# Kernel tuning notes

Hardware: AMD Instinct MI355X
Metric: run time of the kernel (lower is better)

## Reference

```python
import jax, jax.numpy as jnp
import numpy as np

V, D, C, H = 32, 128, 2048, 8
B, M = 8, 2048
HD = D // H


def rms_norm(x, scale):
    # Whole-tensor (per-batch) RMS over dims (1,2), as in the source (quirky but faithful).
    Bx, Mx, Dx = x.shape
    fr = jnp.sqrt(jnp.sum(x * x, axis=(1, 2))) * (Mx * Dx) ** -0.5  # (B,)
    raw = x / fr[:, None, None]
    return scale[:Mx, :][None, :, :] * raw


def rope_tables(Mx):
    i = jnp.arange(D // 2, dtype=jnp.float32)
    # NOTE: faithful to source: exponent uses (i-1), not i.
    base = jnp.power(10000.0, -2.0 * (i - 1.0) / D)  # (D/2,)
    pos = jnp.arange(Mx, dtype=jnp.float32)
    ang = pos[:, None] * base[None, :]  # (M, D/2)
    return jnp.cos(ang), jnp.sin(ang)


def apply_rope(t, cos, sin):
    # Equivalent to bmm with the block-diagonal 2x2 rotation matrices:
    # out[2i]   =  t[2i]*cos + t[2i+1]*sin
    # out[2i+1] = -t[2i]*sin + t[2i+1]*cos
    te, to = t[..., 0::2], t[..., 1::2]
    oe = te * cos + to * sin
    oo = -te * sin + to * cos
    return jnp.stack([oe, oo], axis=-1).reshape(t.shape)


def mha(q, k, v, in_w, in_b, out_w, out_b):
    Bx, Mx, _ = q.shape
    qp = q @ in_w[:D].T + in_b[:D]
    kp = k @ in_w[D:2 * D].T + in_b[D:2 * D]
    vp = v @ in_w[2 * D:].T + in_b[2 * D:]
    qh = qp.reshape(Bx, Mx, H, HD).transpose(0, 2, 1, 3)
    kh = kp.reshape(Bx, Mx, H, HD).transpose(0, 2, 1, 3)
    vh = vp.reshape(Bx, Mx, H, HD).transpose(0, 2, 1, 3)
    scores = jnp.einsum('bhqd,bhkd->bhqk', qh, kh) / jnp.sqrt(jnp.float32(HD))
    causal = jnp.tril(jnp.ones((Mx, Mx), dtype=bool))
    scores = jnp.where(causal[None, None], scores, -jnp.inf)
    probs = jax.nn.softmax(scores, axis=-1)  # dropout=0.1 in train mode; eval here
    o = jnp.einsum('bhqk,bhkd->bhqd', probs, vh)
    o = o.transpose(0, 2, 1, 3).reshape(Bx, Mx, D)
    return o @ out_w.T + out_b


def setup_inputs():
    key = jax.random.key(0)
    ks = jax.random.split(key, 12)
    s = 0.02
    return {
        'idx': jax.random.randint(ks[0], (B, M), 0, V),
        'targets': jax.random.randint(ks[1], (B, M), 0, V),
        'emb': jax.random.normal(ks[2], (V, D), jnp.float32) * s,
        'rms_scale': jnp.ones((C, D), jnp.float32),
        'Wq': jax.random.normal(ks[3], (D, D), jnp.float32) * s,
        'Wk': jax.random.normal(ks[4], (D, D), jnp.float32) * s,
        'Wv': jax.random.normal(ks[5], (D, D), jnp.float32) * s,
        'in_proj_w': jax.random.normal(ks[6], (3 * D, D), jnp.float32) * s,
        'in_proj_b': jnp.zeros((3 * D,), jnp.float32),
        'out_proj_w': jax.random.normal(ks[7], (D, D), jnp.float32) * s,
        'out_proj_b': jnp.zeros((D,), jnp.float32),
        'lin_w': jax.random.normal(ks[8], (D, D), jnp.float32) * s,
        'lin_b': jnp.zeros((D,), jnp.float32),
        'out_w': jax.random.normal(ks[9], (V, D), jnp.float32) * s,
        'out_b': jnp.zeros((V,), jnp.float32),
    }


def reference(idx, targets, emb, rms_scale, Wq, Wk, Wv, in_proj_w, in_proj_b,
              out_proj_w, out_proj_b, lin_w, lin_b, out_w, out_b):
    x = emb[idx]                                  # (B, M, D)
    x = rms_norm(x, rms_scale)
    Q = x @ Wq.T
    K = x @ Wk.T
    Vv = x @ Wv.T
    cos, sin = rope_tables(x.shape[1])
    q_out = apply_rope(Q, cos, sin)
    k_out = apply_rope(K, cos, sin)
    v_out = apply_rope(Vv, cos, sin)              # source rotates V too (faithful)
    x = x + mha(q_out, k_out, v_out, in_proj_w, in_proj_b, out_proj_w, out_proj_b)
    x = rms_norm(x, rms_scale)
    x = x + jax.nn.relu(x @ lin_w.T + lin_b)
    logits = x @ out_w.T + out_b                  # (B, M, V)
    logp = jax.nn.log_softmax(logits, axis=-1)
    nll = -jnp.take_along_axis(logp, targets[..., None], axis=-1)[..., 0]
    loss = jnp.mean(nll)
    return logits, loss
```

## Files before the change

kernel.cpp:

```cpp
#include <hip/hip_runtime.h>
#include <hip/hip_bf16.h>
#include <math.h>

#define Vv   32
#define Dd   128
#define Hh   8
#define Bb   8
#define Mm   2048
#define BM   (Bb*Mm)
#define NEL  (BM*Dd)
#define XNS  140
#define QKS  396

typedef _Float16 half4_t __attribute__((ext_vector_type(4)));
typedef _Float16 half8_t __attribute__((ext_vector_type(8)));
typedef __fp16   fp16x2  __attribute__((ext_vector_type(2)));
typedef float    float4_t __attribute__((ext_vector_type(4)));
#define MFMA16 __builtin_amdgcn_mfma_f32_16x16x16f16
#define MFMA32 __builtin_amdgcn_mfma_f32_16x16x32_f16

#if __has_builtin(__builtin_amdgcn_exp2f)
__device__ __forceinline__ float fexp2(float x) { return __builtin_amdgcn_exp2f(x); }
#else
__device__ __forceinline__ float fexp2(float x) { return __expf(x * 0.6931471805599453f); }
#endif

__global__ __launch_bounds__(256) void front_kernel(const float* __restrict__ Wq,
                                                    const float* __restrict__ Wk,
                                                    const float* __restrict__ Wv,
                                                    const float* __restrict__ in_w,
                                                    const float* __restrict__ out_pw,
                                                    const float* __restrict__ lin_w,
                                                    const float* __restrict__ out_w,
                                                    _Float16* __restrict__ Wh,
                                                    float* __restrict__ cosT,
                                                    float* __restrict__ sinT,
                                                    const int* __restrict__ idx,
                                                    const float* __restrict__ emb,
                                                    _Float16* __restrict__ Xh,
                                                    float* __restrict__ partials,
                                                    float* __restrict__ lossOut) {
    __shared__ float wsum[4];
    if (blockIdx.x < 1040) {
        if (blockIdx.x == 0 && threadIdx.x == 0) lossOut[0] = 0.f;
        int gid = blockIdx.x * 256 + threadIdx.x;
        if (gid < 135168) {
            const float* src;
            int i;
            if (gid < 131072) {
                int seg = gid >> 14; i = gid & 16383;
                src = seg == 0 ? Wq : seg == 1 ? Wk : seg == 2 ? Wv :
                      seg < 6 ? in_w + (size_t)(seg - 3) * 16384 :
                      seg == 6 ? out_pw : lin_w;
            } else { src = out_w; i = gid - 131072; }
            int tile = i >> 8, within = i & 255;
            int nt = tile >> 3, kk = tile & 7;
            int r = within >> 4, cc = within & 15;
            Wh[gid] = (_Float16)src[(nt * 16 + r) * 128 + kk * 16 + cc];
        } else {
            int rid = gid - 135168;
            int i = rid & 63, m = rid >> 6;
            float ex = -2.0f * ((float)i - 1.0f) / 128.0f;
            float basef = expf(ex * 9.210340371976184f);
            float ang = (float)m * basef;
            cosT[rid] = cosf(ang);
            sinT[rid] = sinf(ang);
        }
    } else {
        int blk = blockIdx.x - 1040;
        int gid = blk * 256 + threadIdx.x;
        int token = gid >> 5, t4 = gid & 31;
        float4 x = *(const float4*)(emb + (size_t)idx[token] * 128 + t4 * 4);
        half4_t o;
        o[0] = (_Float16)x.x; o[1] = (_Float16)x.y; o[2] = (_Float16)x.z; o[3] = (_Float16)x.w;
        *(half4_t*)(Xh + (size_t)gid * 4) = o;
        float v = x.x * x.x + x.y * x.y + x.z * x.z + x.w * x.w;
        #pragma unroll
        for (int off = 32; off; off >>= 1) v += __shfl_xor(v, off);
        int lane = threadIdx.x & 63, wave = threadIdx.x >> 6;
        if (lane == 0) wsum[wave] = v;
        __syncthreads();
        if (threadIdx.x == 0) partials[blk] = wsum[0] + wsum[1] + wsum[2] + wsum[3];
    }
}

__global__ __launch_bounds__(512, 4) void gemm_qkvproj_kernel(const _Float16* __restrict__ xh,
                                                              const float* __restrict__ scale,
                                                              const float* __restrict__ part1,
                                                              const _Float16* __restrict__ Whqkv,
                                                              const _Float16* __restrict__ Whin,
                                                              const float* __restrict__ in_b,
                                                              const float* __restrict__ cosT,
                                                              const float* __restrict__ sinT,
                                                              _Float16* __restrict__ xnh,
                                                              _Float16* __restrict__ Qp,
                                                              _Float16* __restrict__ Kp,
                                                              _Float16* __restrict__ Vp) {
    __shared__ _Float16 xn[32 * XNS];
    __shared__ _Float16 qkv[32 * QKS];
    __shared__ float wsum0[8];
    int tid = threadIdx.x;
    int row0 = blockIdx.x * 32;
    {
        float v = (tid < 256) ? part1[(row0 >> 11) * 256 + tid] : 0.f;
        #pragma unroll
        for (int off = 32; off; off >>= 1) v += __shfl_xor(v, off);
        if ((tid & 63) == 0) wsum0[tid >> 6] = v;
    }
    __syncthreads();
    float iv = 512.0f / sqrtf(((wsum0[0] + wsum0[1]) + (wsum0[2] + wsum0[3])) +
                              ((wsum0[4] + wsum0[5]) + (wsum0[6] + wsum0[7])));
    {
        int rw = tid >> 4, c8 = (tid & 15) * 8;
        int m = (row0 + rw) & (Mm - 1);
        half8_t x8 = *(const half8_t*)(xh + (size_t)(row0 + rw) * 128 + c8);
        const float* sp = scale + (size_t)m * 128 + c8;
        float4 s0 = *(const float4*)sp;
        float4 s1 = *(const float4*)(sp + 4);
        half8_t o8;
        o8[0] = (_Float16)((float)x8[0] * iv * s0.x);
        o8[1] = (_Float16)((float)x8[1] * iv * s0.y);
        o8[2] = (_Float16)((float)x8[2] * iv * s0.z);
        o8[3] = (_Float16)((float)x8[3] * iv * s0.w);
        o8[4] = (_Float16)((float)x8[4] * iv * s1.x);
        o8[5] = (_Float16)((float)x8[5] * iv * s1.y);
        o8[6] = (_Float16)((float)x8[6] * iv * s1.z);
        o8[7] = (_Float16)((float)x8[7] * iv * s1.w);
        *(half8_t*)(xn + rw * XNS + c8) = o8;
        *(half8_t*)(xnh + (size_t)(row0 + rw) * 128 + c8) = o8;
    }
    __syncthreads();
    int wave = tid >> 6, lane = tid & 63;
    int r = lane & 15, c = lane >> 4;
    int nb = wave * 48;
    int aoff = c * 8;
    int boff = r * 16 + (c & 1) * 8;
    int bsel = c >> 1;
    {
        float4_t acc[2][3];
        #pragma unroll
        for (int rt = 0; rt < 2; rt++)
            #pragma unroll
            for (int t = 0; t < 3; t++) acc[rt][t] = (float4_t){0.f, 0.f, 0.f, 0.f};
        #pragma unroll
        for (int kk = 0; kk < 4; kk++) {
            half8_t a0 = *(const half8_t*)(xn + r * XNS + kk * 32 + aoff);
            half8_t a1 = *(const half8_t*)(xn + (16 + r) * XNS + kk * 32 + aoff);
            half8_t wf[3];
            #pragma unroll
            for (int t = 0; t < 3; t++)
                wf[t] = *(const half8_t*)(Whqkv + ((wave * 3 + t) * 8 + kk * 2 + bsel) * 256 + boff);
            #pragma unroll
            for (int t = 0; t < 3; t++) {
                acc[0][t] = MFMA32(a0, wf[t], acc[0][t], 0, 0, 0);
                acc[1][t] = MFMA32(a1, wf[t], acc[1][t], 0, 0, 0);
            }
        }
        #pragma unroll
        for (int rt = 0; rt < 2; rt++) {
            #pragma unroll
            for (int t = 0; t < 3; t++) {
                int n = nb + t * 16 + r;
                int ci = (n & 127) >> 1;
                #pragma unroll
                for (int reg = 0; reg < 4; reg++) {
                    int m2 = (row0 + rt * 16 + 4 * c + reg) & (Mm - 1);
                    float v = acc[rt][t][reg];
                    float vp = __shfl_xor(v, 1);
                    float cs = cosT[m2 * 64 + ci], sn = sinT[m2 * 64 + ci];
                    v = (n & 1) ? (-vp * sn + v * cs) : (v * cs + vp * sn);
                    qkv[(rt * 16 + 4 * c + reg) * QKS + n] = (_Float16)v;
                }
            }
        }
    }
    __syncthreads();
    {
        int seg_lo = nb >> 7;
        int seg_hi = (nb + 32) >> 7;
        float4_t acc[2][3];
        #pragma unroll
        for (int rt = 0; rt < 2; rt++)
            #pragma unroll
            for (int t = 0; t < 3; t++) acc[rt][t] = (float4_t){0.f, 0.f, 0.f, 0.f};
        #pragma unroll
        for (int kk = 0; kk < 4; kk++) {
            half8_t al0 = *(const half8_t*)(qkv + r * QKS + seg_lo * 128 + kk * 32 + aoff);
            half8_t al1 = *(const half8_t*)(qkv + (16 + r) * QKS + seg_lo * 128 + kk * 32 + aoff);
            half8_t ah0 = *(const half8_t*)(qkv + r * QKS + seg_hi * 128 + kk * 32 + aoff);
            half8_t ah1 = *(const half8_t*)(qkv + (16 + r) * QKS + seg_hi * 128 + kk * 32 + aoff);
            #pragma unroll
            for (int t = 0; t < 3; t++) {
                int colg = nb + t * 16;
                int seg = colg >> 7;
                int ntl = (colg & 127) >> 4;
                half8_t wf = *(const half8_t*)(Whin + ((seg * 8 + ntl) * 8 + kk * 2 + bsel) * 256 + boff);
                bool lo = (seg == seg_lo);
                acc[0][t] = MFMA32(lo ? al0 : ah0, wf, acc[0][t], 0, 0, 0);
                acc[1][t] = MFMA32(lo ? al1 : ah1, wf, acc[1][t], 0, 0, 0);
            }
        }
        int bb = row0 >> 11;
        #pragma unroll
        for (int rt = 0; rt < 2; rt++) {
            int t16 = ((row0 + rt * 16) & 2047) >> 4;
            #pragma unroll
            for (int t = 0; t < 3; t++) {
                int colg = nb + t * 16;
                int seg = colg >> 7;
                int h = (colg & 127) >> 4;
                size_t tb = ((size_t)(bb * 8 + h) * 128 + t16) * 256;
                float bv = in_b[colg + r];
                _Float16* dst = seg == 0 ? Qp : seg == 1 ? Kp : Vp;
                #pragma unroll
                for (int reg = 0; reg < 4; reg++) {
                    float v = acc[rt][t][reg] + bv;
                    int key = 4 * c + reg;
                    if (seg < 2) dst[tb + key * 16 + r] = (_Float16)v;
                    else         dst[tb + r * 16 + key] = (_Float16)v;
                }
            }
        }
    }
}

__global__ __launch_bounds__(512, 4) void gemm_ep1_kernel(const _Float16* __restrict__ Oh,
                                                          const _Float16* __restrict__ W6,
                                                          const float* __restrict__ bias,
                                                          const _Float16* __restrict__ xnh,
                                                          _Float16* __restrict__ xresh,
                                                          float* __restrict__ partials) {
    __shared__ _Float16 At[32 * XNS];
    int tid = threadIdx.x;
    int row0 = blockIdx.x * 32;
    {
        int rw = tid >> 4, c8 = (tid & 15) * 8;
        *(half8_t*)(At + rw * XNS + c8) = *(const half8_t*)(Oh + (size_t)(row0 + rw) * 128 + c8);
    }
    __syncthreads();
    int wave = tid >> 6, lane = tid & 63;
    int r = lane & 15, c = lane >> 4;
    int aoff = c * 8;
    int boff = r * 16 + (c & 1) * 8;
    int bsel = c >> 1;
    int n0 = wave * 16;
    float4_t acc[2];
    acc[0] = (float4_t){0.f, 0.f, 0.f, 0.f};
    acc[1] = (float4_t){0.f, 0.f, 0.f, 0.f};
    #pragma unroll
    for (int kk = 0; kk < 4; kk++) {
        half8_t a0 = *(const half8_t*)(At + r * XNS + kk * 32 + aoff);
        half8_t a1 = *(const half8_t*)(At + (16 + r) * XNS + kk * 32 + aoff);
        half8_t wf = *(const half8_t*)(W6 + (wave * 8 + kk * 2 + bsel) * 256 + boff);
        acc[0] = MFMA32(a0, wf, acc[0], 0, 0, 0);
        acc[1] = MFMA32(a1, wf, acc[1], 0, 0, 0);
    }
    float lssq = 0.f;
    int n = n0 + r;
    float bv = bias[n];
    #pragma unroll
    for (int rt = 0; rt < 2; rt++) {
        #pragma unroll
        for (int reg = 0; reg < 4; reg++) {
            int row = row0 + rt * 16 + 4 * c + reg;
            float v = acc[rt][reg] + bv + (float)xnh[(size_t)row * 128 + n];
            lssq += v * v;
            xresh[(size_t)row * 128 + n] = (_Float16)v;
        }
    }
    #pragma unroll
    for (int off = 32; off; off >>= 1) lssq += __shfl_xor(lssq, off);
    __shared__ float wsum[8];
    if (lane == 0) wsum[wave] = lssq;
    __syncthreads();
    if (tid == 0) partials[blockIdx.x] = ((wsum[0] + wsum[1]) + (wsum[2] + wsum[3])) +
                                        ((wsum[4] + wsum[5]) + (wsum[6] + wsum[7]));
}

__global__ __launch_bounds__(512, 4) void gemm_ep2_kernel(const _Float16* __restrict__ xresh,
                                                          const float* __restrict__ scale,
                                                          const float* __restrict__ part2,
                                                          const _Float16* __restrict__ W7,
                                                          const float* __restrict__ bias,
                                                          _Float16* __restrict__ ffoh) {
    __shared__ _Float16 At[32 * XNS];
    int tid = threadIdx.x;
    int row0 = blockIdx.x * 32;
    float pv = part2[(row0 >> 11) * 64 + (tid & 63)];
    #pragma unroll
    for (int off = 32; off; off >>= 1) pv += __shfl_xor(pv, off);
    float iv = 512.0f / sqrtf(pv);
    {
        int rw = tid >> 4, c8 = (tid & 15) * 8;
        int m = (row0 + rw) & (Mm - 1);
        half8_t x8 = *(const half8_t*)(xresh + (size_t)(row0 + rw) * 128 + c8);
        const float* sp = scale + (size_t)m * 128 + c8;
        float4 s0 = *(const float4*)sp;
        float4 s1 = *(const float4*)(sp + 4);
        half8_t o8;
        o8[0] = (_Float16)((float)x8[0] * iv * s0.x);
        o8[1] = (_Float16)((float)x8[1] * iv * s0.y);
        o8[2] = (_Float16)((float)x8[2] * iv * s0.z);
        o8[3] = (_Float16)((float)x8[3] * iv * s0.w);
        o8[4] = (_Float16)((float)x8[4] * iv * s1.x);
        o8[5] = (_Float16)((float)x8[5] * iv * s1.y);
        o8[6] = (_Float16)((float)x8[6] * iv * s1.z);
        o8[7] = (_Float16)((float)x8[7] * iv * s1.w);
        *(half8_t*)(At + rw * XNS + c8) = o8;
    }
    __syncthreads();
    int wave = tid >> 6, lane = tid & 63;
    int r = lane & 15, c = lane >> 4;
    int aoff = c * 8;
    int boff = r * 16 + (c & 1) * 8;
    int bsel = c >> 1;
    int n0 = wave * 16;
    float4_t acc[2];
    acc[0] = (float4_t){0.f, 0.f, 0.f, 0.f};
    acc[1] = (float4_t){0.f, 0.f, 0.f, 0.f};
    #pragma unroll
    for (int kk = 0; kk < 4; kk++) {
        half8_t a0 = *(const half8_t*)(At + r * XNS + kk * 32 + aoff);
        half8_t a1 = *(const half8_t*)(At + (16 + r) * XNS + kk * 32 + aoff);
        half8_t wf = *(const half8_t*)(W7 + (wave * 8 + kk * 2 + bsel) * 256 + boff);
        acc[0] = MFMA32(a0, wf, acc[0], 0, 0, 0);
        acc[1] = MFMA32(a1, wf, acc[1], 0, 0, 0);
    }
    int n = n0 + r;
    float bv = bias[n];
    #pragma unroll
    for (int rt = 0; rt < 2; rt++) {
        #pragma unroll
        for (int reg = 0; reg < 4; reg++) {
            int row = row0 + rt * 16 + 4 * c + reg;
            float v = fmaxf(acc[rt][reg] + bv, 0.f) + (float)xresh[(size_t)row * 128 + n];
            ffoh[(size_t)row * 128 + n] = (_Float16)v;
        }
    }
}

__device__ __forceinline__ half4_t attn_exps(float4_t st, float& ls) {
    float p0 = fexp2(st[0]), p1 = fexp2(st[1]);
    float p2 = fexp2(st[2]), p3 = fexp2(st[3]);
    ls += (p0 + p1) + (p2 + p3);
    fp16x2 lo = __builtin_amdgcn_cvt_pkrtz(p0, p1);
    fp16x2 hi = __builtin_amdgcn_cvt_pkrtz(p2, p3);
    half4_t pf;
    pf[0] = (_Float16)lo[0]; pf[1] = (_Float16)lo[1];
    pf[2] = (_Float16)hi[0]; pf[3] = (_Float16)hi[1];
    return pf;
}
__device__ __forceinline__ half4_t attn_exps_masked(float4_t st, float& ls, int r, int c) {
    float p0 = (4 * c + 0 <= r) ? fexp2(st[0]) : 0.f;
    float p1 = (4 * c + 1 <= r) ? fexp2(st[1]) : 0.f;
    float p2 = (4 * c + 2 <= r) ? fexp2(st[2]) : 0.f;
    float p3 = (4 * c + 3 <= r) ? fexp2(st[3]) : 0.f;
    ls += (p0 + p1) + (p2 + p3);
    fp16x2 lo = __builtin_amdgcn_cvt_pkrtz(p0, p1);
    fp16x2 hi = __builtin_amdgcn_cvt_pkrtz(p2, p3);
    half4_t pf;
    pf[0] = (_Float16)lo[0]; pf[1] = (_Float16)lo[1];
    pf[2] = (_Float16)hi[0]; pf[3] = (_Float16)hi[1];
    return pf;
}

__global__ __launch_bounds__(256) void attn_kernel(const _Float16* __restrict__ Qp,
                                                   const _Float16* __restrict__ Kp,
                                                   const _Float16* __restrict__ Vp,
                                                   _Float16* __restrict__ Oh) {
    __shared__ float mrg[2][10][64];
    int wave = threadIdx.x >> 6, lane = threadIdx.x & 63;
    int pair = blockIdx.x * 2 + (wave >> 1);
    int split = wave & 1;
    int qa = pair & 63, bh = pair >> 6, qb = 127 - qa;
    int r = lane & 15, c = lane >> 4;
    int lofs = r * 16 + 4 * c;
    const _Float16* Kb = Kp + (size_t)bh * 32768 + lofs;
    const _Float16* Vb = Vp + (size_t)bh * 32768 + lofs;
    const _Float16* Qb = Qp + (size_t)bh * 32768 + lofs;
    half4_t qfa = *(const half4_t*)(Qb + qa * 256);
    half4_t qfb = *(const half4_t*)(Qb + qb * 256);
    const _Float16 qscale = (_Float16)0.36067376f;
    qfa *= qscale;
    qfb *= qscale;
    float4_t zero = {0.f, 0.f, 0.f, 0.f};
    float4_t oa = zero, ob = zero;
    float lsa = 0.f, lsb = 0.f;

    for (int kt = split; kt < qa; kt += 2) {
        half4_t k0 = *(const half4_t*)(Kb + (size_t)kt * 256);
        half4_t v0 = *(const half4_t*)(Vb + (size_t)kt * 256);
        float4_t sa = MFMA16(k0, qfa, zero, 0, 0, 0);
        float4_t sb = MFMA16(k0, qfb, zero, 0, 0, 0);
        half4_t pa = attn_exps(sa, lsa);
        half4_t pb = attn_exps(sb, lsb);
        oa = MFMA16(pa, v0, oa, 0, 0, 0);
        ob = MFMA16(pb, v0, ob, 0, 0, 0);
    }
    if ((qa & 1) == split) {
        half4_t k0 = *(const half4_t*)(Kb + (size_t)qa * 256);
        half4_t v0 = *(const half4_t*)(Vb + (size_t)qa * 256);
        float4_t sa = MFMA16(k0, qfa, zero, 0, 0, 0);
        float4_t sb = MFMA16(k0, qfb, zero, 0, 0, 0);
        half4_t pa = attn_exps_masked(sa, lsa, r, c);
        half4_t pb = attn_exps(sb, lsb);
        oa = MFMA16(pa, v0, oa, 0, 0, 0);
        ob = MFMA16(pb, v0, ob, 0, 0, 0);
    }
    {
        int s = qa + 1;
        if ((s & 1) != split) s++;
        for (int kt = s; kt < qb; kt += 2) {
            half4_t k0 = *(const half4_t*)(Kb + (size_t)kt * 256);
            half4_t v0 = *(const half4_t*)(Vb + (size_t)kt * 256);
            float4_t sb = MFMA16(k0, qfb, zero, 0, 0, 0);
            half4_t pb = attn_exps(sb, lsb);
            ob = MFMA16(pb, v0, ob, 0, 0, 0);
        }
    }
    if ((qb & 1) == split) {
        half4_t k0 = *(const half4_t*)(Kb + (size_t)qb * 256);
        half4_t v0 = *(const half4_t*)(Vb + (size_t)qb * 256);
        float4_t sb = MFMA16(k0, qfb, zero, 0, 0, 0);
        half4_t pb = attn_exps_masked(sb, lsb, r, c);
        ob = MFMA16(pb, v0, ob, 0, 0, 0);
    }
    int pib = wave >> 1;
    if (split == 1) {
        #pragma unroll
        for (int i = 0; i < 4; i++) {
            mrg[pib][i][lane] = oa[i];
            mrg[pib][4 + i][lane] = ob[i];
        }
        mrg[pib][8][lane] = lsa;
        mrg[pib][9][lane] = lsb;
    }
    __syncthreads();
    if (split == 0) {
        #pragma unroll
        for (int i = 0; i < 4; i++) {
            oa[i] += mrg[pib][i][lane];
            ob[i] += mrg[pib][4 + i][lane];
        }
        lsa += mrg[pib][8][lane];
        lsb += mrg[pib][9][lane];
        lsa += __shfl_xor(lsa, 16); lsa += __shfl_xor(lsa, 32);
        lsb += __shfl_xor(lsb, 16); lsb += __shfl_xor(lsb, 32);
        int b = bh >> 3, h = bh & 7;
        #pragma unroll
        for (int reg = 0; reg < 4; reg++) {
            float la = __shfl(lsa, 4 * c + reg);
            float lb = __shfl(lsb, 4 * c + reg);
            Oh[(size_t)(b * Mm + qa * 16 + 4 * c + reg) * 128 + h * 16 + r] = (_Float16)(oa[reg] / la);
            Oh[(size_t)(b * Mm + qb * 16 + 4 * c + reg) * 128 + h * 16 + r] = (_Float16)(ob[reg] / lb);
        }
    }
}

__global__ __launch_bounds__(256) void logits_loss_kernel(const _Float16* __restrict__ Xh,
                                                          const _Float16* __restrict__ Wo16,
                                                          const float* __restrict__ bo,
                                                          const int* __restrict__ targets,
                                                          float* __restrict__ logits,
                                                          float* __restrict__ lossOut) {
    __shared__ _Float16 At[64 * XNS];
    __shared__ float wn[4];
    int tid = threadIdx.x;
    int rowb = blockIdx.x * 64;
    #pragma unroll
    for (int it = 0; it < 4; it++) {
        int idx = tid + it * 256;
        int rw = idx >> 4, c8 = (idx & 15) * 8;
        *(half8_t*)(At + rw * XNS + c8) = *(const half8_t*)(Xh + (size_t)(rowb + rw) * 128 + c8);
    }
    __syncthreads();
    int wave = tid >> 6, lane = tid & 63;
    int r = lane & 15, c = lane >> 4;
    int aoff = c * 8;
    int boff = r * 16 + (c & 1) * 8;
    int bsel = c >> 1;
    int row0 = rowb + wave * 16;
    half8_t af[4];
    #pragma unroll
    for (int kk = 0; kk < 4; kk++)
        af[kk] = *(const half8_t*)(At + (wave * 16 + r) * XNS + kk * 32 + aoff);
    float4_t acc[2];
    acc[0] = (float4_t){0.f, 0.f, 0.f, 0.f};
    acc[1] = (float4_t){0.f, 0.f, 0.f, 0.f};
    #pragma unroll
    for (int kk = 0; kk < 4; kk++) {
        #pragma unroll
        for (int t = 0; t < 2; t++) {
            half8_t wf = *(const half8_t*)(Wo16 + (t * 8 + kk * 2 + bsel) * 256 + boff);
            acc[t] = MFMA32(af[kk], wf, acc[t], 0, 0, 0);
        }
    }
    float b0 = bo[r], b1 = bo[r + 16];
    float nll_s = 0.f;
    #pragma unroll
    for (int reg = 0; reg < 4; reg++) {
        int row = row0 + 4 * c + reg;
        float l0 = acc[0][reg] + b0;
        float l1 = acc[1][reg] + b1;
        logits[(size_t)row * 32 + r] = l0;
        logits[(size_t)row * 32 + 16 + r] = l1;
        float mx = fmaxf(l0, l1);
        #pragma unroll
        for (int off = 8; off; off >>= 1) mx = fmaxf(mx, __shfl_xor(mx, off));
        float se = __expf(l0 - mx) + __expf(l1 - mx);
        #pragma unroll
        for (int off = 8; off; off >>= 1) se += __shfl_xor(se, off);
        int tgt = targets[row];
        float sel = (tgt & 16) ? l1 : l0;
        float tval = __shfl(sel, (lane & 48) | (tgt & 15));
        nll_s += logf(se) + mx - tval;
    }
    nll_s += __shfl_xor(nll_s, 16);
    nll_s += __shfl_xor(nll_s, 32);
    if (lane == 0) wn[wave] = nll_s;
    __syncthreads();
    if (tid == 0) atomicAdd(lossOut, ((wn[0] + wn[1]) + (wn[2] + wn[3])) * (1.0f / (float)BM));
}

extern "C" void kernel_launch(void* const* d_in, const int* in_sizes, int n_in,
                              void* d_out, int out_size, void* d_ws, size_t ws_size,
                              hipStream_t stream) {
    const int*   idx       = (const int*)d_in[0];
    const int*   targets   = (const int*)d_in[1];
    const float* emb       = (const float*)d_in[2];
    const float* rms_scale = (const float*)d_in[3];
    const float* Wq        = (const float*)d_in[4];
    const float* Wk        = (const float*)d_in[5];
    const float* Wv        = (const float*)d_in[6];
    const float* in_w      = (const float*)d_in[7];
    const float* in_b      = (const float*)d_in[8];
    const float* out_pw    = (const float*)d_in[9];
    const float* out_pb    = (const float*)d_in[10];
    const float* lin_w     = (const float*)d_in[11];
    const float* lin_b     = (const float*)d_in[12];
    const float* out_w     = (const float*)d_in[13];
    const float* out_b     = (const float*)d_in[14];
    float* out = (float*)d_out;
    float* lossOut = out + (size_t)BM * Vv;

    char* base = (char*)d_ws;
    const size_t MB = 1024 * 1024;
    _Float16* xh16  = (_Float16*)base;
    _Float16* xnh   = (_Float16*)(base + 4 * MB);
    _Float16* Oh    = (_Float16*)(base + 8 * MB);
    _Float16* xresh = (_Float16*)(base + 12 * MB);
    _Float16* ffoh  = (_Float16*)(base + 16 * MB);
    _Float16* Qp    = (_Float16*)(base + 20 * MB);
    _Float16* Kp    = (_Float16*)(base + 24 * MB);
    _Float16* Vp    = (_Float16*)(base + 28 * MB);
    float*    cosT  = (float*)(base + 32 * MB);
    float*    sinT  = cosT + Mm * 64;
    float*    part1 = sinT + Mm * 64;
    float*    part2 = part1 + 2048;
    _Float16* Wh    = (_Float16*)(part2 + 512);

    front_kernel<<<1040 + 2048, 256, 0, stream>>>(Wq, Wk, Wv, in_w, out_pw, lin_w, out_w,
                                                  Wh, cosT, sinT, idx, emb, xh16, part1, lossOut);

    gemm_qkvproj_kernel<<<BM / 32, 512, 0, stream>>>(xh16, rms_scale, part1,
                                                     Wh, Wh + 3 * 16384, in_b,
                                                     cosT, sinT, xnh, Qp, Kp, Vp);

    attn_kernel<<<4096 / 2, 256, 0, stream>>>(Qp, Kp, Vp, Oh);

    gemm_ep1_kernel<<<BM / 32, 512, 0, stream>>>(Oh, Wh + 6 * 16384, out_pb, xnh, xresh, part2);
    gemm_ep2_kernel<<<BM / 32, 512, 0, stream>>>(xresh, rms_scale, part2, Wh + 7 * 16384, lin_b, ffoh);

    logits_loss_kernel<<<BM / 64, 256, 0, stream>>>(ffoh, Wh + 131072, out_b, targets, out, lossOut);
}
```

Before: 154.6 us.

## Fuse logits/loss into FFN epilogue and gather embeddings directly in QKV kernel

The FFN epilogue kernel now keeps its output tile in shared memory and computes logits, log-softmax and NLL in the same block, which removes the separate logits kernel and the ffoh round trip through global memory. The front kernel no longer writes a half-precision copy of the embeddings. The QKV kernel instead gathers fp32 embedding rows by index itself. This cuts one launch and two intermediate global buffers, at the cost of extra shared memory and only two active waves during the logits phase.

```diff
diff --git a/kernel.cpp b/kernel.cpp
--- a/kernel.cpp
+++ b/kernel.cpp
@@ -37,7 +37,6 @@
                                                     float* __restrict__ sinT,
                                                     const int* __restrict__ idx,
                                                     const float* __restrict__ emb,
-                                                    _Float16* __restrict__ Xh,
                                                     float* __restrict__ partials,
                                                     float* __restrict__ lossOut) {
     __shared__ float wsum[4];
@@ -71,9 +70,6 @@
         int gid = blk * 256 + threadIdx.x;
         int token = gid >> 5, t4 = gid & 31;
         float4 x = *(const float4*)(emb + (size_t)idx[token] * 128 + t4 * 4);
-        half4_t o;
-        o[0] = (_Float16)x.x; o[1] = (_Float16)x.y; o[2] = (_Float16)x.z; o[3] = (_Float16)x.w;
-        *(half4_t*)(Xh + (size_t)gid * 4) = o;
         float v = x.x * x.x + x.y * x.y + x.z * x.z + x.w * x.w;
         #pragma unroll
         for (int off = 32; off; off >>= 1) v += __shfl_xor(v, off);
@@ -84,7 +80,8 @@
     }
 }
 
-__global__ __launch_bounds__(512, 4) void gemm_qkvproj_kernel(const _Float16* __restrict__ xh,
+__global__ __launch_bounds__(512, 4) void gemm_qkvproj_kernel(const int* __restrict__ idx,
+                                                              const float* __restrict__ emb,
                                                               const float* __restrict__ scale,
                                                               const float* __restrict__ part1,
                                                               const _Float16* __restrict__ Whqkv,
@@ -113,19 +110,21 @@
     {
         int rw = tid >> 4, c8 = (tid & 15) * 8;
         int m = (row0 + rw) & (Mm - 1);
-        half8_t x8 = *(const half8_t*)(xh + (size_t)(row0 + rw) * 128 + c8);
+        const float* ep = emb + (size_t)idx[row0 + rw] * 128 + c8;
+        float4 xa = *(const float4*)ep;
+        float4 xb = *(const float4*)(ep + 4);
         const float* sp = scale + (size_t)m * 128 + c8;
         float4 s0 = *(const float4*)sp;
         float4 s1 = *(const float4*)(sp + 4);
         half8_t o8;
-        o8[0] = (_Float16)((float)x8[0] * iv * s0.x);
-        o8[1] = (_Float16)((float)x8[1] * iv * s0.y);
-        o8[2] = (_Float16)((float)x8[2] * iv * s0.z);
-        o8[3] = (_Float16)((float)x8[3] * iv * s0.w);
-        o8[4] = (_Float16)((float)x8[4] * iv * s1.x);
-        o8[5] = (_Float16)((float)x8[5] * iv * s1.y);
-        o8[6] = (_Float16)((float)x8[6] * iv * s1.z);
-        o8[7] = (_Float16)((float)x8[7] * iv * s1.w);
+        o8[0] = (_Float16)(xa.x * iv * s0.x);
+        o8[1] = (_Float16)(xa.y * iv * s0.y);
+        o8[2] = (_Float16)(xa.z * iv * s0.z);
+        o8[3] = (_Float16)(xa.w * iv * s0.w);
+        o8[4] = (_Float16)(xb.x * iv * s1.x);
+        o8[5] = (_Float16)(xb.y * iv * s1.y);
+        o8[6] = (_Float16)(xb.z * iv * s1.z);
+        o8[7] = (_Float16)(xb.w * iv * s1.w);
         *(half8_t*)(xn + rw * XNS + c8) = o8;
         *(half8_t*)(xnh + (size_t)(row0 + rw) * 128 + c8) = o8;
     }
@@ -277,13 +276,19 @@
                                         ((wsum[4] + wsum[5]) + (wsum[6] + wsum[7]));
 }
 
-__global__ __launch_bounds__(512, 4) void gemm_ep2_kernel(const _Float16* __restrict__ xresh,
-                                                          const float* __restrict__ scale,
-                                                          const float* __restrict__ part2,
-                                                          const _Float16* __restrict__ W7,
-                                                          const float* __restrict__ bias,
-                                                          _Float16* __restrict__ ffoh) {
+__global__ __launch_bounds__(512, 4) void gemm_ep2_logits_kernel(const _Float16* __restrict__ xresh,
+                                                                 const float* __restrict__ scale,
+                                                                 const float* __restrict__ part2,
+                                                                 const _Float16* __restrict__ W7,
+                                                                 const float* __restrict__ bias,
+                                                                 const _Float16* __restrict__ Wo16,
+                                                                 const float* __restrict__ bo,
+                                                                 const int* __restrict__ targets,
+                                                                 float* __restrict__ logits,
+                                                                 float* __restrict__ lossOut) {
     __shared__ _Float16 At[32 * XNS];
+    __shared__ _Float16 Ao[32 * XNS];
+    __shared__ float wn[2];
     int tid = threadIdx.x;
     int row0 = blockIdx.x * 32;
     float pv = part2[(row0 >> 11) * 64 + (tid & 63)];
@@ -333,10 +338,55 @@
         #pragma unroll
         for (int reg = 0; reg < 4; reg++) {
             int row = row0 + rt * 16 + 4 * c + reg;
+            int rowl = rt * 16 + 4 * c + reg;
             float v = fmaxf(acc[rt][reg] + bv, 0.f) + (float)xresh[(size_t)row * 128 + n];
-            ffoh[(size_t)row * 128 + n] = (_Float16)v;
-        }
-    }
+            Ao[rowl * XNS + n] = (_Float16)v;
+        }
+    }
+    __syncthreads();
+    if (wave < 2) {
+        int rloc = wave * 16;
+        half8_t af[4];
+        #pragma unroll
+        for (int kk = 0; kk < 4; kk++)
+            af[kk] = *(const half8_t*)(Ao + (rloc + r) * XNS + kk * 32 + aoff);
+        float4_t lacc[2];
+        lacc[0] = (float4_t){0.f, 0.f, 0.f, 0.f};
+        lacc[1] = (float4_t){0.f, 0.f, 0.f, 0.f};
+        #pragma unroll
+        for (int kk = 0; kk < 4; kk++) {
+            #pragma unroll
+            for (int t = 0; t < 2; t++) {
+                half8_t wf = *(const half8_t*)(Wo16 + (t * 8 + kk * 2 + bsel) * 256 + boff);
+                lacc[t] = MFMA32(af[kk], wf, lacc[t], 0, 0, 0);
+            }
+        }
+        float b0 = bo[r], b1 = bo[r + 16];
+        float nll_s = 0.f;
+        #pragma unroll
+        for (int reg = 0; reg < 4; reg++) {
+            int row = row0 + rloc + 4 * c + reg;
+            float l0 = lacc[0][reg] + b0;
+            float l1 = lacc[1][reg] + b1;
+            logits[(size_t)row * 32 + r] = l0;
+            logits[(size_t)row * 32 + 16 + r] = l1;
+            float mx = fmaxf(l0, l1);
+            #pragma unroll
+            for (int off = 8; off; off >>= 1) mx = fmaxf(mx, __shfl_xor(mx, off));
+            float se = __expf(l0 - mx) + __expf(l1 - mx);
+            #pragma unroll
+            for (int off = 8; off; off >>= 1) se += __shfl_xor(se, off);
+            int tgt = targets[row];
+            float sel = (tgt & 16) ? l1 : l0;
+            float tval = __shfl(sel, (lane & 48) | (tgt & 15));
+            nll_s += logf(se) + mx - tval;
+        }
+        nll_s += __shfl_xor(nll_s, 16);
+        nll_s += __shfl_xor(nll_s, 32);
+        if (lane == 0) wn[wave] = nll_s;
+    }
+    __syncthreads();
+    if (tid == 0) atomicAdd(lossOut, (wn[0] + wn[1]) * (1.0f / (float)BM));
 }
 
 __device__ __forceinline__ half4_t attn_exps(float4_t st, float& ls) {
@@ -457,71 +507,6 @@
     }
 }
 
-__global__ __launch_bounds__(256) void logits_loss_kernel(const _Float16* __restrict__ Xh,
-                                                          const _Float16* __restrict__ Wo16,
-                                                          const float* __restrict__ bo,
-                                                          const int* __restrict__ targets,
-                                                          float* __restrict__ logits,
-                                                          float* __restrict__ lossOut) {
-    __shared__ _Float16 At[64 * XNS];
-    __shared__ float wn[4];
-    int tid = threadIdx.x;
-    int rowb = blockIdx.x * 64;
-    #pragma unroll
-    for (int it = 0; it < 4; it++) {
-        int idx = tid + it * 256;
-        int rw = idx >> 4, c8 = (idx & 15) * 8;
-        *(half8_t*)(At + rw * XNS + c8) = *(const half8_t*)(Xh + (size_t)(rowb + rw) * 128 + c8);
-    }
-    __syncthreads();
-    int wave = tid >> 6, lane = tid & 63;
-    int r = lane & 15, c = lane >> 4;
-    int aoff = c * 8;
-    int boff = r * 16 + (c & 1) * 8;
-    int bsel = c >> 1;
-    int row0 = rowb + wave * 16;
-    half8_t af[4];
-    #pragma unroll
-    for (int kk = 0; kk < 4; kk++)
-        af[kk] = *(const half8_t*)(At + (wave * 16 + r) * XNS + kk * 32 + aoff);
-    float4_t acc[2];
-    acc[0] = (float4_t){0.f, 0.f, 0.f, 0.f};
-    acc[1] = (float4_t){0.f, 0.f, 0.f, 0.f};
-    #pragma unroll
-    for (int kk = 0; kk < 4; kk++) {
-        #pragma unroll
-        for (int t = 0; t < 2; t++) {
-            half8_t wf = *(const half8_t*)(Wo16 + (t * 8 + kk * 2 + bsel) * 256 + boff);
-            acc[t] = MFMA32(af[kk], wf, acc[t], 0, 0, 0);
-        }
-    }
-    float b0 = bo[r], b1 = bo[r + 16];
-    float nll_s = 0.f;
-    #pragma unroll
-    for (int reg = 0; reg < 4; reg++) {
-        int row = row0 + 4 * c + reg;
-        float l0 = acc[0][reg] + b0;
-        float l1 = acc[1][reg] + b1;
-        logits[(size_t)row * 32 + r] = l0;
-        logits[(size_t)row * 32 + 16 + r] = l1;
-        float mx = fmaxf(l0, l1);
-        #pragma unroll
-        for (int off = 8; off; off >>= 1) mx = fmaxf(mx, __shfl_xor(mx, off));
-        float se = __expf(l0 - mx) + __expf(l1 - mx);
-        #pragma unroll
-        for (int off = 8; off; off >>= 1) se += __shfl_xor(se, off);
-        int tgt = targets[row];
-        float sel = (tgt & 16) ? l1 : l0;
-        float tval = __shfl(sel, (lane & 48) | (tgt & 15));
-        nll_s += logf(se) + mx - tval;
-    }
-    nll_s += __shfl_xor(nll_s, 16);
-    nll_s += __shfl_xor(nll_s, 32);
-    if (lane == 0) wn[wave] = nll_s;
-    __syncthreads();
-    if (tid == 0) atomicAdd(lossOut, ((wn[0] + wn[1]) + (wn[2] + wn[3])) * (1.0f / (float)BM));
-}
-
 extern "C" void kernel_launch(void* const* d_in, const int* in_sizes, int n_in,
                               void* d_out, int out_size, void* d_ws, size_t ws_size,
                               hipStream_t stream) {
@@ -545,11 +530,9 @@
 
     char* base = (char*)d_ws;
     const size_t MB = 1024 * 1024;
-    _Float16* xh16  = (_Float16*)base;
     _Float16* xnh   = (_Float16*)(base + 4 * MB);
     _Float16* Oh    = (_Float16*)(base + 8 * MB);
     _Float16* xresh = (_Float16*)(base + 12 * MB);
-    _Float16* ffoh  = (_Float16*)(base + 16 * MB);
     _Float16* Qp    = (_Float16*)(base + 20 * MB);
     _Float16* Kp    = (_Float16*)(base + 24 * MB);
     _Float16* Vp    = (_Float16*)(base + 28 * MB);
@@ -560,16 +543,18 @@
     _Float16* Wh    = (_Float16*)(part2 + 512);
 
     front_kernel<<<1040 + 2048, 256, 0, stream>>>(Wq, Wk, Wv, in_w, out_pw, lin_w, out_w,
-                                                  Wh, cosT, sinT, idx, emb, xh16, part1, lossOut);
-
-    gemm_qkvproj_kernel<<<BM / 32, 512, 0, stream>>>(xh16, rms_scale, part1,
+                                                  Wh, cosT, sinT, idx, emb, part1, lossOut);
+
+    gemm_qkvproj_kernel<<<BM / 32, 512, 0, stream>>>(idx, emb, rms_scale, part1,
                                                      Wh, Wh + 3 * 16384, in_b,
                                                      cosT, sinT, xnh, Qp, Kp, Vp);
 
     attn_kernel<<<4096 / 2, 256, 0, stream>>>(Qp, Kp, Vp, Oh);
 
     gemm_ep1_kernel<<<BM / 32, 512, 0, stream>>>(Oh, Wh + 6 * 16384, out_pb, xnh, xresh, part2);
-    gemm_ep2_kernel<<<BM / 32, 512, 0, stream>>>(xresh, rms_scale, part2, Wh + 7 * 16384, lin_b, ffoh);
-
-    logits_loss_kernel<<<BM / 64, 256, 0, stream>>>(ffoh, Wh + 131072, out_b, targets, out, lossOut);
-}
+
+    gemm_ep2_logits_kernel<<<BM / 32, 512, 0, stream>>>(xresh, rms_scale, part2,
+                                                        Wh + 7 * 16384, lin_b,
+                                                        Wh + 131072, out_b, targets,
+                                                        out, lossOut);
+}
```

After: 150.1 us. 2.9% less time.
